# Performance work log

Measured on AMD Instinct MI355X. Metric: run time of the kernel, lower is better.

The kernel has to match this reference:

```python
import jax, jax.numpy as jnp
import numpy as np


def _morlet_kernel_bank(n_scales: int, n: int) -> np.ndarray:
    """Build the per-scale Morlet wavelets (the module's fallback CWT),
    zero-padded into a common buffer of length Lmax so that slicing a
    'same' convolution with the padded kernel matches np.convolve(sig, w,
    mode='same') for each original kernel length."""
    Lmax = min(8 * n_scales, n)
    bank = np.zeros((n_scales, Lmax), dtype=np.float32)
    for i, s in enumerate(range(1, n_scales + 1)):
        L = min(8 * s, n)
        t = np.linspace(-4.0 * s, 4.0 * s, L)
        w = np.exp(-t ** 2 / (2.0 * s ** 2)) * np.cos(5.0 * t / s)
        w = w / np.sqrt(s)
        off = (Lmax - 1) // 2 - (L - 1) // 2  # align 'same'-conv centers
        bank[i, off:off + L] = w.astype(np.float32)
    return bank


def _cwt_energy(x, n_scales):
    # x: [batch, time]
    n = x.shape[1]
    bank = _morlet_kernel_bank(n_scales, n)          # [S, Lmax], static
    Lmax = bank.shape[1]
    # lax.conv does cross-correlation; flip kernel to get true convolution
    k = jnp.asarray(bank[:, ::-1].copy())[:, None, :]  # [S, 1, Lmax]
    pl = Lmax - 1 - (Lmax - 1) // 2
    pr = (Lmax - 1) // 2
    coef = jax.lax.conv_general_dilated(
        x[:, None, :], k, window_strides=(1,), padding=[(pl, pr)],
        dimension_numbers=('NCH', 'OIH', 'NCH'))   # [batch, S, time]
    return jnp.mean(coef * coef, axis=-1)            # [batch, S]


def setup_inputs() -> dict:
    key = jax.random.key(0)
    k1, k2 = jax.random.split(key)
    x = jax.random.normal(k1, (128, 8192), dtype=jnp.float32)
    scale_weights = jax.random.normal(k2, (32,), dtype=jnp.float32)
    return {"x": x, "scale_weights": scale_weights}


def reference(x, scale_weights):
    n_scales = scale_weights.shape[0]
    energy = _cwt_energy(x, n_scales)                # [batch, n_scales]
    return energy * jax.nn.softmax(scale_weights)
```

## Files before the change

### kernel.cpp

```cpp
#include <hip/hip_runtime.h>
#include <hip/hip_bf16.h>
#include <math.h>

#define NT      8192
#define NS      32
#define KTAPS   256
#define TQ      2048
#define XELEM   (TQ + KTAPS)
#define XSTRIDE 2320
#define NCOPY   4

typedef __attribute__((ext_vector_type(8)))  short bf16x8;
typedef __attribute__((ext_vector_type(4)))  short short4v;
typedef __attribute__((ext_vector_type(16))) float f32x16;
typedef __attribute__((ext_vector_type(4)))  float float4v;

__global__ void bank_kernel(unsigned short* __restrict__ abf) {
    int e   = blockIdx.x * 256 + threadIdx.x;
    int kap = e >> 9;
    int l   = (e >> 3) & 63;
    int j   = e & 7;
    int sc  = (l & 31) + 1;
    int k   = kap * 16 + ((l >> 5) << 3) + j;
    int L   = 8 * sc;
    int u   = k - (128 - 4 * sc);
    float val = 0.f;
    if (u >= 0 && u < L) {
        float tau = fmaf(8.0f / (float)(L - 1), (float)u, -4.0f);
        val = expf(-0.5f * tau * tau) * cosf(5.0f * tau) / sqrtf((float)sc);
    }
    __hip_bfloat16 bv = __float2bfloat16(val);
    abf[e] = *reinterpret_cast<unsigned short*>(&bv);
}

__global__ __launch_bounds__(512, 2)
void cwt_mfma_kernel(const float* __restrict__ x,
                     const unsigned short* __restrict__ abf,
                     float* __restrict__ part)
{
    __shared__ unsigned short XL[NCOPY * XSTRIDE];
    __shared__ float redE[8 * 2 * 16];

    const int tid = threadIdx.x;
    const int b   = blockIdx.x >> 2;
    const int qt  = blockIdx.x & 3;
    const int T0  = qt * TQ;

    const float* xrow = x + (size_t)b * NT;
    for (int q = tid; q < XELEM / 4; q += 512) {
        float v[8];
        #pragma unroll
        for (int h = 0; h < 2; ++h) {
            int xi = T0 + 4 * (q + h) - 128;
            float4v f;
            if (xi >= 0 && xi <= NT - 4) f = *reinterpret_cast<const float4v*>(xrow + xi);
            else { f[0] = 0.f; f[1] = 0.f; f[2] = 0.f; f[3] = 0.f; }
            v[4 * h + 0] = f[0]; v[4 * h + 1] = f[1];
            v[4 * h + 2] = f[2]; v[4 * h + 3] = f[3];
        }
        unsigned short ub[8];
        #pragma unroll
        for (int i = 0; i < 8; ++i) {
            __hip_bfloat16 t = __float2bfloat16(v[i]);
            ub[i] = *reinterpret_cast<unsigned short*>(&t);
        }
        #pragma unroll
        for (int c = 0; c < NCOPY; ++c) {
            short4v w;
            w[0] = (short)ub[c + 0]; w[1] = (short)ub[c + 1];
            w[2] = (short)ub[c + 2]; w[3] = (short)ub[c + 3];
            *reinterpret_cast<short4v*>(&XL[c * XSTRIDE + 4 * q]) = w;
        }
    }
    __syncthreads();

    const int wv   = tid >> 6;
    const int lane = tid & 63;
    const int n    = lane & 31;
    const int hh   = lane >> 5;

    const unsigned short* xc = &XL[(n & 3) * XSTRIDE];
    const int ibase = 256 * wv + 4 * (n >> 2) + 8 * hh;

    f32x16 zz;
    #pragma unroll
    for (int r = 0; r < 16; ++r) zz[r] = 0.f;
    f32x16 acc[8];
    #pragma unroll
    for (int m = 0; m < 8; ++m) acc[m] = zz;

    bf16x8 ring[16];
    #define LOADB(D) ({                                                              \
        short4v lo_ = *reinterpret_cast<const short4v*>(xc + ibase + 16 * (D));      \
        short4v hi_ = *reinterpret_cast<const short4v*>(xc + ibase + 16 * (D) + 4);  \
        __builtin_shufflevector(lo_, hi_, 0, 1, 2, 3, 4, 5, 6, 7); })

    #pragma unroll
    for (int D = 0; D < 14; ++D) ring[D] = LOADB(D);

    const unsigned short* ap = abf + lane * 8;
    #pragma unroll
    for (int kap = 0; kap < 16; ++kap) {
        bf16x8 afrag = *reinterpret_cast<const bf16x8*>(ap + kap * 512);
        ring[(kap + 14) & 15] = LOADB(kap + 14);
        #pragma unroll
        for (int m = 0; m < 8; ++m)
            acc[m] = __builtin_amdgcn_mfma_f32_32x32x16_bf16(
                         afrag, ring[(kap + 2 * m) & 15], acc[m], 0, 0, 0);
    }

    float ep[16];
    #pragma unroll
    for (int r = 0; r < 16; ++r) {
        float s = 0.f;
        #pragma unroll
        for (int m = 0; m < 8; ++m) s = fmaf(acc[m][r], acc[m][r], s);
        ep[r] = s;
    }
    #pragma unroll
    for (int r = 0; r < 16; ++r) {
        ep[r] += __shfl_xor(ep[r], 16);
        ep[r] += __shfl_xor(ep[r], 8);
        ep[r] += __shfl_xor(ep[r], 4);
        ep[r] += __shfl_xor(ep[r], 2);
        ep[r] += __shfl_xor(ep[r], 1);
    }
    if ((lane & 31) == 0) {
        #pragma unroll
        for (int r = 0; r < 16; ++r) redE[(wv * 2 + hh) * 16 + r] = ep[r];
    }
    __syncthreads();
    if (tid < 32) {
        int s  = tid;
        int r  = (s >> 3) * 4 + (s & 3);
        int hi = (s >> 2) & 1;
        float tot = 0.f;
        #pragma unroll
        for (int w = 0; w < 8; ++w) tot += redE[(w * 2 + hi) * 16 + r];
        part[(b * 4 + qt) * 32 + s] = tot;
    }
}

__global__ void combine_kernel(const float* __restrict__ part,
                               const float* __restrict__ sw,
                               float* __restrict__ out) {
    int g = blockIdx.x * 256 + threadIdx.x;
    if (g >= 128 * 32) return;
    int b = g >> 5, s = g & 31;
    float mx = -1e30f;
    for (int i = 0; i < NS; ++i) mx = fmaxf(mx, sw[i]);
    float den = 0.f;
    for (int i = 0; i < NS; ++i) den += expf(sw[i] - mx);
    float soft = expf(sw[s] - mx) / den;
    float tot = 0.f;
    #pragma unroll
    for (int qv = 0; qv < 4; ++qv) tot += part[(b * 4 + qv) * 32 + s];
    out[g] = tot * (1.0f / (float)NT) * soft;
}

extern "C" void kernel_launch(void* const* d_in, const int* in_sizes, int n_in,
                              void* d_out, int out_size, void* d_ws, size_t ws_size,
                              hipStream_t stream) {
    const float* x  = (const float*)d_in[0];
    const float* sw = (const float*)d_in[1];
    float* out = (float*)d_out;

    unsigned short* abf = (unsigned short*)d_ws;
    float* part = (float*)((char*)d_ws + 16384);

    hipLaunchKernelGGL(bank_kernel, dim3(32), dim3(256), 0, stream, abf);
    hipLaunchKernelGGL(cwt_mfma_kernel, dim3(512), dim3(512), 0, stream, x, abf, part);
    hipLaunchKernelGGL(combine_kernel, dim3(16), dim3(256), 0, stream, part, sw, out);
}
```

Before: 28.23 us.

## Fuse bank generation and softmax combine into the main CWT kernel

Each block now builds the bf16 Morlet filter bank in shared memory and reads afrag fragments from LDS rather than global memory. The separate combine kernel is removed: blocks compute the softmax weights and atomically add their scaled partial energies into the output, which a memset zeroes first. This cuts two kernel launches and the workspace round-trip, but every block repeats the bank transcendentals and adds 16 KB of LDS, which could lower occupancy.

```diff
diff --git a/kernel.cpp b/kernel.cpp
--- a/kernel.cpp
+++ b/kernel.cpp
@@ -15,29 +15,12 @@
 typedef __attribute__((ext_vector_type(16))) float f32x16;
 typedef __attribute__((ext_vector_type(4)))  float float4v;
 
-__global__ void bank_kernel(unsigned short* __restrict__ abf) {
-    int e   = blockIdx.x * 256 + threadIdx.x;
-    int kap = e >> 9;
-    int l   = (e >> 3) & 63;
-    int j   = e & 7;
-    int sc  = (l & 31) + 1;
-    int k   = kap * 16 + ((l >> 5) << 3) + j;
-    int L   = 8 * sc;
-    int u   = k - (128 - 4 * sc);
-    float val = 0.f;
-    if (u >= 0 && u < L) {
-        float tau = fmaf(8.0f / (float)(L - 1), (float)u, -4.0f);
-        val = expf(-0.5f * tau * tau) * cosf(5.0f * tau) / sqrtf((float)sc);
-    }
-    __hip_bfloat16 bv = __float2bfloat16(val);
-    abf[e] = *reinterpret_cast<unsigned short*>(&bv);
-}
-
 __global__ __launch_bounds__(512, 2)
-void cwt_mfma_kernel(const float* __restrict__ x,
-                     const unsigned short* __restrict__ abf,
-                     float* __restrict__ part)
+void cwt_fused_kernel(const float* __restrict__ x,
+                      const float* __restrict__ sw,
+                      float* __restrict__ out)
 {
+    __shared__ unsigned short AW[8192];
     __shared__ unsigned short XL[NCOPY * XSTRIDE];
     __shared__ float redE[8 * 2 * 16];
 
@@ -45,6 +28,32 @@
     const int b   = blockIdx.x >> 2;
     const int qt  = blockIdx.x & 3;
     const int T0  = qt * TQ;
+
+    {
+        unsigned short vb[16];
+        #pragma unroll
+        for (int i = 0; i < 16; ++i) {
+            int e   = tid * 16 + i;
+            int kap = e >> 9;
+            int l   = (e >> 3) & 63;
+            int j   = e & 7;
+            int sc  = (l & 31) + 1;
+            int k   = kap * 16 + ((l >> 5) << 3) + j;
+            int L   = 8 * sc;
+            int u   = k - (128 - 4 * sc);
+            float val = 0.f;
+            if (u >= 0 && u < L) {
+                float tau = fmaf(8.0f / (float)(L - 1), (float)u, -4.0f);
+                val = expf(-0.5f * tau * tau) * cosf(5.0f * tau) / sqrtf((float)sc);
+            }
+            __hip_bfloat16 bv = __float2bfloat16(val);
+            vb[i] = *reinterpret_cast<unsigned short*>(&bv);
+        }
+        #pragma unroll
+        for (int h = 0; h < 4; ++h)
+            *reinterpret_cast<short4v*>(&AW[tid * 16 + 4 * h]) =
+                *reinterpret_cast<short4v*>(&vb[4 * h]);
+    }
 
     const float* xrow = x + (size_t)b * NT;
     for (int q = tid; q < XELEM / 4; q += 512) {
@@ -98,7 +107,7 @@
     #pragma unroll
     for (int D = 0; D < 14; ++D) ring[D] = LOADB(D);
 
-    const unsigned short* ap = abf + lane * 8;
+    const unsigned short* ap = AW + lane * 8;
     #pragma unroll
     for (int kap = 0; kap < 16; ++kap) {
         bf16x8 afrag = *reinterpret_cast<const bf16x8*>(ap + kap * 512);
@@ -137,25 +146,13 @@
         float tot = 0.f;
         #pragma unroll
         for (int w = 0; w < 8; ++w) tot += redE[(w * 2 + hi) * 16 + r];
-        part[(b * 4 + qt) * 32 + s] = tot;
+        float mx = -1e30f;
+        for (int i = 0; i < NS; ++i) mx = fmaxf(mx, sw[i]);
+        float den = 0.f;
+        for (int i = 0; i < NS; ++i) den += expf(sw[i] - mx);
+        float soft = expf(sw[s] - mx) / den;
+        atomicAdd(&out[b * NS + s], tot * (1.0f / (float)NT) * soft);
     }
-}
-
-__global__ void combine_kernel(const float* __restrict__ part,
-                               const float* __restrict__ sw,
-                               float* __restrict__ out) {
-    int g = blockIdx.x * 256 + threadIdx.x;
-    if (g >= 128 * 32) return;
-    int b = g >> 5, s = g & 31;
-    float mx = -1e30f;
-    for (int i = 0; i < NS; ++i) mx = fmaxf(mx, sw[i]);
-    float den = 0.f;
-    for (int i = 0; i < NS; ++i) den += expf(sw[i] - mx);
-    float soft = expf(sw[s] - mx) / den;
-    float tot = 0.f;
-    #pragma unroll
-    for (int qv = 0; qv < 4; ++qv) tot += part[(b * 4 + qv) * 32 + s];
-    out[g] = tot * (1.0f / (float)NT) * soft;
 }
 
 extern "C" void kernel_launch(void* const* d_in, const int* in_sizes, int n_in,
@@ -164,11 +161,6 @@
     const float* x  = (const float*)d_in[0];
     const float* sw = (const float*)d_in[1];
     float* out = (float*)d_out;
-
-    unsigned short* abf = (unsigned short*)d_ws;
-    float* part = (float*)((char*)d_ws + 16384);
-
-    hipLaunchKernelGGL(bank_kernel, dim3(32), dim3(256), 0, stream, abf);
-    hipLaunchKernelGGL(cwt_mfma_kernel, dim3(512), dim3(512), 0, stream, x, abf, part);
-    hipLaunchKernelGGL(combine_kernel, dim3(16), dim3(256), 0, stream, part, sw, out);
+    hipMemsetAsync(out, 0, (size_t)out_size * sizeof(float), stream);
+    hipLaunchKernelGGL(cwt_fused_kernel, dim3(512), dim3(512), 0, stream, x, sw, out);
 }
```

Result: slower. 37.33 us (+32.2%).
